# Kernel optimization log

Measured on AMD Instinct MI355X. Metric: run time of the kernel, lower is better.

The kernel has to match this reference:

```python
import jax, jax.numpy as jnp
import numpy as np
from math import factorial

ZETA = [1, 2, 3, 4]          # configs['zeta']=4 -> range(1,5)
NZETA = len(ZETA)
NRAD = 16
NLAMBDA = 2
NAT = 4000
NEDGE = 100000
ZMAX = max(ZETA)


def _make_lxlylz(zmax):
    tr, fn = [], []
    for s in range(zmax + 1):
        for lx in range(s + 1):
            for ly in range(s - lx + 1):
                lz = s - lx - ly
                tr.append((lx, ly, lz))
                fn.append(factorial(s) / (factorial(lx) * factorial(ly) * factorial(lz)))
    return np.asarray(tr, np.int32), np.asarray(fn, np.float32)


def setup_inputs() -> dict:
    key = jax.random.key(0)
    k1, k2, k3, k4 = jax.random.split(key, 4)
    rij = jax.random.normal(k1, (NEDGE, 3), dtype=jnp.float32)
    rij_unit = rij / jnp.linalg.norm(rij, axis=-1, keepdims=True)
    radial_ij = jax.random.uniform(k2, (NEDGE, NRAD, NZETA + 1), dtype=jnp.float32)
    lambda_weights = jax.random.normal(k3, (NLAMBDA,), dtype=jnp.float32)
    first_atom_idx = jnp.sort(jax.random.randint(k4, (NEDGE,), 0, NAT, dtype=jnp.int32))
    tr, fn = _make_lxlylz(ZMAX)
    return {
        "rij_unit": rij_unit,
        "radial_ij": radial_ij,
        "lambda_weights": lambda_weights,
        "fact_norm": jnp.asarray(fn),
        "first_atom_idx": first_atom_idx,
        "lxlylz": jnp.asarray(tr),
        "lxlylz_sum": jnp.asarray(tr.sum(axis=-1).astype(np.int32)),
        "nat": NAT,
    }


def reference(rij_unit, radial_ij, lambda_weights, fact_norm,
              first_atom_idx, lxlylz, lxlylz_sum, nat):
    # angular monomials g_ij_lxlylz : [E, L]
    lf = lxlylz.astype(jnp.float32)
    g_ij = jnp.prod(rij_unit[:, None, :] ** lf[None, :, :], axis=-1) * fact_norm[None, :]
    # lambda^(lx+ly+lz) : [n_lambda, L]
    lam = lambda_weights[:, None] ** lxlylz_sum.astype(jnp.float32)[None, :]
    # two-body radial descriptor: segment-sum of last radial channel -> [nat, Nrad]
    radial_i = jax.ops.segment_sum(radial_ij[:, :, -1], first_atom_idx, num_segments=nat)
    feats = [radial_i]
    for r_idx, z in enumerate(ZETA):
        # gather-compute: [E, Nrad, L]
        g = jnp.einsum('ej,ek->ejk', radial_ij[:, :, r_idx], g_ij)
        # scatter-reduce over neighbors of each central atom -> [nat, Nrad, L]
        g_i = jax.ops.segment_sum(g, first_atom_idx, num_segments=nat)
        # three-body power contraction with lambda weights, norm 2^(1-z)
        gi3 = jnp.einsum('njk,lk->njl', g_i * g_i, lam) * jnp.float32(2.0 ** (1.0 - z))
        feats.append(gi3.reshape(nat, -1))
    return jnp.concatenate(feats, axis=-1)  # [nat, Nrad*(1 + n_lambda*nzeta)]
```

## Files before the change

kernel.cpp:

```cpp
#include <hip/hip_runtime.h>

#define NRAD 16
#define NCH  5
#define NMON 35
#define OUTW 144

__global__ __launch_bounds__(256) void seg_offsets(
    const int* __restrict__ idx, int* __restrict__ seg, int E, int nat)
{
    int e = blockIdx.x * blockDim.x + threadIdx.x;
    if (e >= E) return;
    if (e == 0) {
        const int b = idx[0];
        for (int n = 0; n <= b; ++n) seg[n] = 0;
    } else {
        const int a = idx[e - 1], b = idx[e];
        for (int n = a + 1; n <= b; ++n) seg[n] = e;
    }
    if (e == E - 1) {
        const int a = idx[E - 1];
        for (int n = a + 1; n <= nat; ++n) seg[n] = E;
    }
}

__device__ __forceinline__ void edge_body(
    float x, float y, float z, float rad, float c4,
    float acc[NMON], float& acc2)
{
    const float x2 = x * x, x3 = x2 * x, x4 = x2 * x2;
    const float y2 = y * y, y3 = y2 * y, y4 = y2 * y2;
    const float z2 = z * z, z3 = z2 * z, z4 = z2 * z2;
    const float xy = x * y, xz = x * z, yz = y * z;

    acc2 += c4;
    acc[0]  += rad;
    acc[1]  = fmaf(rad, z,        acc[1]);
    acc[2]  = fmaf(rad, y,        acc[2]);
    acc[3]  = fmaf(rad, x,        acc[3]);
    acc[4]  = fmaf(rad, z2,       acc[4]);
    acc[5]  = fmaf(rad, yz,       acc[5]);
    acc[6]  = fmaf(rad, y2,       acc[6]);
    acc[7]  = fmaf(rad, xz,       acc[7]);
    acc[8]  = fmaf(rad, xy,       acc[8]);
    acc[9]  = fmaf(rad, x2,       acc[9]);
    acc[10] = fmaf(rad, z3,       acc[10]);
    acc[11] = fmaf(rad, y * z2,   acc[11]);
    acc[12] = fmaf(rad, y2 * z,   acc[12]);
    acc[13] = fmaf(rad, y3,       acc[13]);
    acc[14] = fmaf(rad, x * z2,   acc[14]);
    acc[15] = fmaf(rad, xy * z,   acc[15]);
    acc[16] = fmaf(rad, x * y2,   acc[16]);
    acc[17] = fmaf(rad, x2 * z,   acc[17]);
    acc[18] = fmaf(rad, x2 * y,   acc[18]);
    acc[19] = fmaf(rad, x3,       acc[19]);
    acc[20] = fmaf(rad, z4,       acc[20]);
    acc[21] = fmaf(rad, y * z3,   acc[21]);
    acc[22] = fmaf(rad, y2 * z2,  acc[22]);
    acc[23] = fmaf(rad, y3 * z,   acc[23]);
    acc[24] = fmaf(rad, y4,       acc[24]);
    acc[25] = fmaf(rad, x * z3,   acc[25]);
    acc[26] = fmaf(rad, xy * z2,  acc[26]);
    acc[27] = fmaf(rad, x * y2 * z, acc[27]);
    acc[28] = fmaf(rad, x * y3,   acc[28]);
    acc[29] = fmaf(rad, x2 * z2,  acc[29]);
    acc[30] = fmaf(rad, x2 * yz,  acc[30]);
    acc[31] = fmaf(rad, x2 * y2,  acc[31]);
    acc[32] = fmaf(rad, x3 * z,   acc[32]);
    acc[33] = fmaf(rad, x3 * y,   acc[33]);
    acc[34] = fmaf(rad, x4,       acc[34]);
}

__global__ __launch_bounds__(256) void mbp_main(
    const float* __restrict__ rij_unit,
    const float* __restrict__ radial_ij,
    const float* __restrict__ lambda_w,
    const float* __restrict__ fact_norm,
    const int*   __restrict__ seg,
    float* __restrict__ out,
    int nat)
{
    const int wave = threadIdx.x >> 6;
    const int n = blockIdx.x * 4 + wave;
    if (n >= nat) return;
    const int lane = threadIdx.x & 63;
    const int zi = lane >> 4;
    const int r  = lane & 15;

    const int start = seg[n];
    const int end   = seg[n + 1];

    float acc[NMON];
    #pragma unroll
    for (int l = 0; l < NMON; ++l) acc[l] = 0.f;
    float acc2 = 0.f;

    const int roff = r * NCH + zi;
    const int coff = r * NCH + 4;

    int e = start;
    for (; e + 4 <= end; e += 4) {
        float xs[4], ys[4], zs[4], rd[4], c4[4];
        #pragma unroll
        for (int u = 0; u < 4; ++u) {
            const int ee = e + u;
            xs[u] = rij_unit[ee * 3 + 0];
            ys[u] = rij_unit[ee * 3 + 1];
            zs[u] = rij_unit[ee * 3 + 2];
            rd[u] = radial_ij[ee * (NRAD * NCH) + roff];
            c4[u] = radial_ij[ee * (NRAD * NCH) + coff];
        }
        #pragma unroll
        for (int u = 0; u < 4; ++u)
            edge_body(xs[u], ys[u], zs[u], rd[u], c4[u], acc, acc2);
    }
    for (; e < end; ++e) {
        const float x = rij_unit[e * 3 + 0];
        const float y = rij_unit[e * 3 + 1];
        const float z = rij_unit[e * 3 + 2];
        const float rad = radial_ij[e * (NRAD * NCH) + roff];
        const float c4v = radial_ij[e * (NRAD * NCH) + coff];
        edge_body(x, y, z, rad, c4v, acc, acc2);
    }

    const float l0 = lambda_w[0], l1 = lambda_w[1];
    const float p0[5] = {1.f, l0, l0 * l0, l0 * l0 * l0, (l0 * l0) * (l0 * l0)};
    const float p1[5] = {1.f, l1, l1 * l1, l1 * l1 * l1, (l1 * l1) * (l1 * l1)};
    const int lsum_tab[NMON] = {0, 1,1,1, 2,2,2,2,2,2,
                                3,3,3,3,3,3,3,3,3,3,
                                4,4,4,4,4,4,4,4,4,4,4,4,4,4,4};
    float s0 = 0.f, s1 = 0.f;
    #pragma unroll
    for (int l = 0; l < NMON; ++l) {
        const float v = acc[l] * fact_norm[l];
        const float v2 = v * v;
        s0 = fmaf(v2, p0[lsum_tab[l]], s0);
        s1 = fmaf(v2, p1[lsum_tab[l]], s1);
    }
    const float scale = 1.0f / (float)(1 << zi);
    float* orow = out + (long)n * OUTW;
    orow[16 + zi * 32 + r * 2 + 0] = s0 * scale;
    orow[16 + zi * 32 + r * 2 + 1] = s1 * scale;
    if (zi == 0) orow[r] = acc2;
}

extern "C" void kernel_launch(void* const* d_in, const int* in_sizes, int n_in,
                              void* d_out, int out_size, void* d_ws, size_t ws_size,
                              hipStream_t stream) {
    const float* rij_unit   = (const float*)d_in[0];
    const float* radial_ij  = (const float*)d_in[1];
    const float* lambda_w   = (const float*)d_in[2];
    const float* fact_norm  = (const float*)d_in[3];
    const int*   first_atom = (const int*)d_in[4];
    const int E   = in_sizes[4];
    const int nat = out_size / OUTW;

    int* seg = (int*)d_ws;

    seg_offsets<<<(E + 255) / 256, 256, 0, stream>>>(first_atom, seg, E, nat);
    mbp_main<<<(nat + 3) / 4, 256, 0, stream>>>(rij_unit, radial_ij, lambda_w,
                                                fact_norm, seg, (float*)d_out, nat);
}
```

Measured before the change: 107.7 us.

## Split each atom's edges across a block's waves with LDS staging and reduction

```diff
diff --git a/kernel.cpp b/kernel.cpp
--- a/kernel.cpp
+++ b/kernel.cpp
@@ -4,6 +4,8 @@
 #define NCH  5
 #define NMON 35
 #define OUTW 144
+#define TILE 64
+#define ROWF (NRAD * NCH)
 
 __global__ __launch_bounds__(256) void seg_offsets(
     const int* __restrict__ idx, int* __restrict__ seg, int E, int nat)
@@ -79,12 +81,15 @@
     float* __restrict__ out,
     int nat)
 {
-    const int wave = threadIdx.x >> 6;
-    const int n = blockIdx.x * 4 + wave;
-    if (n >= nat) return;
-    const int lane = threadIdx.x & 63;
-    const int zi = lane >> 4;
-    const int r  = lane & 15;
+    __shared__ float rad_t[TILE * ROWF];
+    __shared__ float rij_t[TILE * 3];
+
+    const int n    = blockIdx.x;
+    const int tid  = threadIdx.x;
+    const int wave = tid >> 6;
+    const int lane = tid & 63;
+    const int zi   = lane >> 4;
+    const int r    = lane & 15;
 
     const int start = seg[n];
     const int end   = seg[n + 1];
@@ -94,33 +99,57 @@
     for (int l = 0; l < NMON; ++l) acc[l] = 0.f;
     float acc2 = 0.f;
 
-    const int roff = r * NCH + zi;
-    const int coff = r * NCH + 4;
+    for (int ts = start; ts < end; ts += TILE) {
+        const int T = min(TILE, end - ts);
 
-    int e = start;
-    for (; e + 4 <= end; e += 4) {
-        float xs[4], ys[4], zs[4], rd[4], c4[4];
+        {
+            const float4* __restrict__ src = (const float4*)(radial_ij + (size_t)ts * ROWF);
+            float4* dst = (float4*)rad_t;
+            const int nf4 = T * (ROWF / 4);
+            for (int i = tid; i < nf4; i += 256) dst[i] = src[i];
+        }
+        for (int i = tid; i < T * 3; i += 256) rij_t[i] = rij_unit[(size_t)ts * 3 + i];
+        __syncthreads();
+
+        for (int j = wave; j < T; j += 4) {
+            const float x   = rij_t[j * 3 + 0];
+            const float y   = rij_t[j * 3 + 1];
+            const float z   = rij_t[j * 3 + 2];
+            const float rad = rad_t[j * ROWF + r * NCH + zi];
+            const float c4  = rad_t[j * ROWF + r * NCH + 4];
+            edge_body(x, y, z, rad, c4, acc, acc2);
+        }
+        __syncthreads();
+    }
+
+    float* red = rad_t;
+    const int region = wave >> 1;
+    const int rbase  = region * (NMON + 1) * 64;
+
+    if (wave & 1) {
         #pragma unroll
-        for (int u = 0; u < 4; ++u) {
-            const int ee = e + u;
-            xs[u] = rij_unit[ee * 3 + 0];
-            ys[u] = rij_unit[ee * 3 + 1];
-            zs[u] = rij_unit[ee * 3 + 2];
-            rd[u] = radial_ij[ee * (NRAD * NCH) + roff];
-            c4[u] = radial_ij[ee * (NRAD * NCH) + coff];
-        }
+        for (int l = 0; l < NMON; ++l) red[rbase + l * 64 + lane] = acc[l];
+        red[rbase + NMON * 64 + lane] = acc2;
+    }
+    __syncthreads();
+    if (!(wave & 1)) {
         #pragma unroll
-        for (int u = 0; u < 4; ++u)
-            edge_body(xs[u], ys[u], zs[u], rd[u], c4[u], acc, acc2);
+        for (int l = 0; l < NMON; ++l) acc[l] += red[rbase + l * 64 + lane];
+        acc2 += red[rbase + NMON * 64 + lane];
     }
-    for (; e < end; ++e) {
-        const float x = rij_unit[e * 3 + 0];
-        const float y = rij_unit[e * 3 + 1];
-        const float z = rij_unit[e * 3 + 2];
-        const float rad = radial_ij[e * (NRAD * NCH) + roff];
-        const float c4v = radial_ij[e * (NRAD * NCH) + coff];
-        edge_body(x, y, z, rad, c4v, acc, acc2);
+    __syncthreads();
+    if (wave == 2) {
+        #pragma unroll
+        for (int l = 0; l < NMON; ++l) red[rbase + l * 64 + lane] = acc[l];
+        red[rbase + NMON * 64 + lane] = acc2;
     }
+    __syncthreads();
+    if (wave != 0) return;
+
+    const int r1base = (NMON + 1) * 64;
+    #pragma unroll
+    for (int l = 0; l < NMON; ++l) acc[l] += red[r1base + l * 64 + lane];
+    acc2 += red[r1base + NMON * 64 + lane];
 
     const float l0 = lambda_w[0], l1 = lambda_w[1];
     const float p0[5] = {1.f, l0, l0 * l0, l0 * l0 * l0, (l0 * l0) * (l0 * l0)};
@@ -157,6 +186,6 @@
     int* seg = (int*)d_ws;
 
     seg_offsets<<<(E + 255) / 256, 256, 0, stream>>>(first_atom, seg, E, nat);
-    mbp_main<<<(nat + 3) / 4, 256, 0, stream>>>(rij_unit, radial_ij, lambda_w,
-                                                fact_norm, seg, (float*)d_out, nat);
+    mbp_main<<<nat, 256, 0, stream>>>(rij_unit, radial_ij, lambda_w,
+                                      fact_norm, seg, (float*)d_out, nat);
 }
```

Result: no change. 106.3 us (-1.3%).
